# Kernel tuning notes

Measured on AMD Instinct MI355X. Metric: run time of the kernel, lower is better.

## Reference

```python
import jax, jax.numpy as jnp
import numpy as np

B, T, H, NH, K = 8, 1024, 1024, 16, 3
HD = H // NH
EPS = 1e-5


def _ln(x, g, b):
    m = jnp.mean(x, axis=-1, keepdims=True)
    v = jnp.mean((x - m) ** 2, axis=-1, keepdims=True)
    return (x - m) * jax.lax.rsqrt(v + EPS) * g + b


def _ffn(x, g, b, w1, b1, w2, b2):
    h = jax.nn.gelu(_ln(x, g, b) @ w1 + b1, approximate=False)
    return h @ w2 + b2


def setup_inputs() -> dict:
    key = jax.random.key(0)
    ks = jax.random.split(key, 10)
    s = 0.02
    d = {}
    d['x'] = jax.random.normal(ks[0], (B, T, H), jnp.float32)
    d['ln1_g'] = jnp.ones((H,), jnp.float32); d['ln1_b'] = jnp.zeros((H,), jnp.float32)
    d['ffn1_w1'] = jax.random.normal(ks[1], (H, 2 * H), jnp.float32) * s
    d['ffn1_b1'] = jnp.zeros((2 * H,), jnp.float32)
    d['ffn1_w2'] = jax.random.normal(ks[2], (2 * H, H), jnp.float32) * s
    d['ffn1_b2'] = jnp.zeros((H,), jnp.float32)
    d['an_g'] = jnp.ones((H,), jnp.float32); d['an_b'] = jnp.zeros((H,), jnp.float32)
    d['qkv_w'] = jax.random.normal(ks[3], (H, 3 * H), jnp.float32) * s
    d['qkv_b'] = jnp.zeros((3 * H,), jnp.float32)
    d['out_w'] = jax.random.normal(ks[4], (H, H), jnp.float32) * s
    d['out_b'] = jnp.zeros((H,), jnp.float32)
    d['cn_g'] = jnp.ones((H,), jnp.float32); d['cn_b'] = jnp.zeros((H,), jnp.float32)
    d['dw_k'] = jax.random.normal(ks[5], (H, 1, K), jnp.float32) * s  # depthwise [O,I/g,K]
    d['dw_b'] = jnp.zeros((H,), jnp.float32)
    d['pw_w'] = jax.random.normal(ks[6], (H, H), jnp.float32) * s  # pointwise [out,in]
    d['pw_b'] = jnp.zeros((H,), jnp.float32)
    d['ln2_g'] = jnp.ones((H,), jnp.float32); d['ln2_b'] = jnp.zeros((H,), jnp.float32)
    d['ffn2_w1'] = jax.random.normal(ks[7], (H, 2 * H), jnp.float32) * s
    d['ffn2_b1'] = jnp.zeros((2 * H,), jnp.float32)
    d['ffn2_w2'] = jax.random.normal(ks[8], (2 * H, H), jnp.float32) * s
    d['ffn2_b2'] = jnp.zeros((H,), jnp.float32)
    return d


def reference(x, ln1_g, ln1_b, ffn1_w1, ffn1_b1, ffn1_w2, ffn1_b2,
              an_g, an_b, qkv_w, qkv_b, out_w, out_b,
              cn_g, cn_b, dw_k, dw_b, pw_w, pw_b,
              ln2_g, ln2_b, ffn2_w1, ffn2_b1, ffn2_w2, ffn2_b2):
    # macaron FFN 1
    x = x + 0.5 * _ffn(x, ln1_g, ln1_b, ffn1_w1, ffn1_b1, ffn1_w2, ffn1_b2)

    # causal self-attention (pre-norm)
    h = _ln(x, an_g, an_b)
    qkv = (h @ qkv_w + qkv_b).reshape(B, T, 3, NH, HD)
    q, k, v = qkv[:, :, 0], qkv[:, :, 1], qkv[:, :, 2]  # [B,T,NH,HD]
    scale = 1.0 / np.sqrt(HD).astype(np.float32)
    scores = jnp.einsum('bqhd,bkhd->bhqk', q, k) * scale  # [B,NH,T,T]
    causal = jnp.tril(jnp.ones((T, T), dtype=bool))
    scores = jnp.where(causal[None, None], scores, -jnp.inf)
    attn = jax.nn.softmax(scores, axis=-1)
    o = jnp.einsum('bhqk,bkhd->bqhd', attn, v).reshape(B, T, H)
    x = x + (o @ out_w + out_b)

    # conv module: LN -> causal depthwise conv(k=3) -> GELU -> pointwise conv
    c = _ln(x, cn_g, cn_b).transpose(0, 2, 1)  # [B,H,T]
    c = jnp.pad(c, ((0, 0), (0, 0), (K - 1, 0)))  # causal left pad
    c = jax.lax.conv_general_dilated(
        c, dw_k, window_strides=(1,), padding='VALID',
        dimension_numbers=('NCH', 'OIH', 'NCH'), feature_group_count=H)
    c = c + dw_b[None, :, None]
    c = jax.nn.gelu(c, approximate=False)
    c = jnp.einsum('oc,bct->bot', pw_w, c) + pw_b[None, :, None]  # 1x1 conv
    x = x + c.transpose(0, 2, 1)

    # macaron FFN 2
    x = x + 0.5 * _ffn(x, ln2_g, ln2_b, ffn2_w1, ffn2_b1, ffn2_w2, ffn2_b2)
    return x
```

## Files before the change

kernel.cpp:

```cpp
#include <hip/hip_runtime.h>
#include <hip/hip_bf16.h>
#include <math.h>

typedef __bf16 bf16;
typedef __bf16 bf16x8 __attribute__((ext_vector_type(8)));
typedef float  f32x4  __attribute__((ext_vector_type(4)));

#define B_   8
#define T_   1024
#define H_   1024
#define MTOK (B_ * T_)

static __device__ __forceinline__ float gelu_f(float x) {
    return 0.5f * x * (1.0f + erff(x * 0.70710678118654752f));
}

static __device__ __forceinline__ void async16(const bf16* g, bf16* l) {
    __builtin_amdgcn_global_load_lds(
        (const __attribute__((address_space(1))) void*)g,
        (__attribute__((address_space(3))) void*)l, 16, 0, 0);
}

__global__ __launch_bounds__(256)
void transpose_cast_k(const float* __restrict__ in, bf16* __restrict__ out,
                      int Kd, int Nd)
{
    __shared__ float tile[32][33];
    int n0 = blockIdx.x * 32;
    int k0 = blockIdx.y * 32;
    int tx = threadIdx.x & 31, ty = threadIdx.x >> 5;
#pragma unroll
    for (int i = 0; i < 32; i += 8)
        tile[ty + i][tx] = in[(size_t)(k0 + ty + i) * Nd + n0 + tx];
    __syncthreads();
#pragma unroll
    for (int i = 0; i < 32; i += 8)
        out[(size_t)(n0 + ty + i) * Kd + k0 + tx] = (bf16)tile[tx][ty + i];
}

__global__ __launch_bounds__(256)
void cast_k(const float* __restrict__ in, bf16* __restrict__ out)
{
    int i = blockIdx.x * 256 + threadIdx.x;
    float4 v = ((const float4*)in)[i];
    bf16* o = out + (size_t)i * 4;
    o[0] = (bf16)v.x; o[1] = (bf16)v.y; o[2] = (bf16)v.z; o[3] = (bf16)v.w;
}

__global__ __launch_bounds__(256)
void transpose_v_k(const bf16* __restrict__ qkv, bf16* __restrict__ vt)
{
    __shared__ bf16 tile[64][72];
    const int t0 = blockIdx.x * 64;
    const int bh = blockIdx.y;
    const int b = bh >> 4, h = bh & 15;
    const int tid = threadIdx.x;
#pragma unroll
    for (int i = 0; i < 2; i++) {
        int c = tid + i * 256;
        int row = c >> 3, ch = (c & 7) << 3;
        *(bf16x8*)(&tile[row][ch]) =
            *(const bf16x8*)(&qkv[(size_t)(b * T_ + t0 + row) * 3072 + 2048 + h * 64 + ch]);
    }
    __syncthreads();
#pragma unroll
    for (int i = 0; i < 2; i++) {
        int c = tid + i * 256;
        int hd = c >> 3, tc = (c & 7) << 3;
        bf16x8 v;
#pragma unroll
        for (int j = 0; j < 8; j++) v[j] = tile[tc + j][hd];
        *(bf16x8*)(&vt[((size_t)bh * 64 + hd) * T_ + t0 + tc]) = v;
    }
}

__global__ __launch_bounds__(256)
void ln_k(const float* __restrict__ x, const float* __restrict__ g,
          const float* __restrict__ b, bf16* __restrict__ out)
{
    int row = blockIdx.x;
    float4 v = ((const float4*)(x + (size_t)row * H_))[threadIdx.x];
    float s  = v.x + v.y + v.z + v.w;
    float s2 = v.x * v.x + v.y * v.y + v.z * v.z + v.w * v.w;
#pragma unroll
    for (int off = 32; off > 0; off >>= 1) {
        s  += __shfl_down(s, off);
        s2 += __shfl_down(s2, off);
    }
    __shared__ float red[8];
    int wave = threadIdx.x >> 6, lane = threadIdx.x & 63;
    if (lane == 0) { red[wave] = s; red[wave + 4] = s2; }
    __syncthreads();
    s  = red[0] + red[1] + red[2] + red[3];
    s2 = red[4] + red[5] + red[6] + red[7];
    float mean = s * (1.0f / H_);
    float var  = s2 * (1.0f / H_) - mean * mean;
    float rstd = rsqrtf(var + 1e-5f);
    int c = threadIdx.x * 4;
    float4 gv = *(const float4*)(g + c);
    float4 bv = *(const float4*)(b + c);
    bf16* o = out + (size_t)row * H_ + c;
    o[0] = (bf16)((v.x - mean) * rstd * gv.x + bv.x);
    o[1] = (bf16)((v.y - mean) * rstd * gv.y + bv.y);
    o[2] = (bf16)((v.z - mean) * rstd * gv.z + bv.z);
    o[3] = (bf16)((v.w - mean) * rstd * gv.w + bv.w);
}

__global__ __launch_bounds__(256)
void dwconv_k(const bf16* __restrict__ cl, const float* __restrict__ kw,
              const float* __restrict__ kb, bf16* __restrict__ out)
{
    size_t idx = (size_t)blockIdx.x * 256 + threadIdx.x;
    int ch = (int)(idx & (H_ - 1));
    int t  = (int)((idx >> 10) & (T_ - 1));
    float acc = kb[ch];
    float w0 = kw[ch * 3 + 0], w1 = kw[ch * 3 + 1], w2 = kw[ch * 3 + 2];
    acc += (float)cl[idx] * w2;
    if (t >= 1) acc += (float)cl[idx - H_] * w1;
    if (t >= 2) acc += (float)cl[idx - 2 * H_] * w0;
    out[idx] = (bf16)gelu_f(acc);
}

template<int EPI>
__global__ __launch_bounds__(256)
void gemm_k(const bf16* __restrict__ A, const bf16* __restrict__ WT,
            const float* __restrict__ bias, const float* __restrict__ res,
            float* __restrict__ outF, bf16* __restrict__ outB,
            int N, int K)
{
    __shared__ __align__(16) bf16 As[2][128 * 32];
    __shared__ __align__(16) bf16 Bs[2][128 * 32];
    const int tid  = threadIdx.x;
    const int wave = tid >> 6;
    const int lane = tid & 63;
    const int quad = lane >> 4;
    const int lr   = lane & 15;
    const int bm = blockIdx.x * 128;
    const int bn = blockIdx.y * 128;
    const int wm = (wave & 1) * 64;
    const int wn = (wave >> 1) * 64;

    const int crow = lane >> 2;
    const int ccol = (lane & 3) << 3;

    f32x4 acc[4][4];
#pragma unroll
    for (int mi = 0; mi < 4; mi++)
#pragma unroll
        for (int ni = 0; ni < 4; ni++)
#pragma unroll
            for (int r = 0; r < 4; r++) acc[mi][ni][r] = 0.f;

    for (int k0 = 0; k0 < K; k0 += 64) {
#pragma unroll
        for (int half = 0; half < 2; half++) {
#pragma unroll
            for (int t = 0; t < 2; t++) {
                const int c = wave * 2 + t;
                async16(&A[(size_t)(bm + c * 16 + crow) * K + k0 + half * 32 + ccol],
                        &As[half][c * 512]);
                async16(&WT[(size_t)(bn + c * 16 + crow) * K + k0 + half * 32 + ccol],
                        &Bs[half][c * 512]);
            }
        }
        __syncthreads();
#pragma unroll
        for (int half = 0; half < 2; half++) {
            bf16x8 af[4], bfr[4];
#pragma unroll
            for (int mi = 0; mi < 4; mi++)
                af[mi] = *(const bf16x8*)(&As[half][(wm + mi * 16 + lr) * 32 + quad * 8]);
#pragma unroll
            for (int ni = 0; ni < 4; ni++)
                bfr[ni] = *(const bf16x8*)(&Bs[half][(wn + ni * 16 + lr) * 32 + quad * 8]);
#pragma unroll
            for (int mi = 0; mi < 4; mi++)
#pragma unroll
                for (int ni = 0; ni < 4; ni++)
                    acc[mi][ni] = __builtin_amdgcn_mfma_f32_16x16x32_bf16(
                        af[mi], bfr[ni], acc[mi][ni], 0, 0, 0);
        }
        __syncthreads();
    }

#pragma unroll
    for (int mi = 0; mi < 4; mi++) {
#pragma unroll
        for (int ni = 0; ni < 4; ni++) {
            int col = bn + wn + ni * 16 + lr;
            float bv = bias[col];
#pragma unroll
            for (int r = 0; r < 4; r++) {
                int row = bm + wm + mi * 16 + quad * 4 + r;
                size_t idx = (size_t)row * N + col;
                float v = acc[mi][ni][r] + bv;
                if (EPI == 0)      outB[idx] = (bf16)gelu_f(v);
                else if (EPI == 1) outB[idx] = (bf16)v;
                else if (EPI == 2) outF[idx] = v + res[idx];
                else               outF[idx] = res[idx] + 0.5f * v;
            }
        }
    }
}

template<int EPI>
__global__ __launch_bounds__(256)
void gemm64_k(const bf16* __restrict__ A, const bf16* __restrict__ WT,
              const float* __restrict__ bias, const float* __restrict__ res,
              float* __restrict__ outF, bf16* __restrict__ outB,
              int N, int K)
{
    __shared__ __align__(16) bf16 As[2][64 * 32];
    __shared__ __align__(16) bf16 Bs[2][128 * 32];
    const int tid  = threadIdx.x;
    const int wave = tid >> 6;
    const int lane = tid & 63;
    const int quad = lane >> 4;
    const int lr   = lane & 15;
    const int bm = blockIdx.x * 64;
    const int bn = blockIdx.y * 128;
    const int wm = (wave & 1) * 32;
    const int wn = (wave >> 1) * 64;

    const int crow = lane >> 2;
    const int ccol = (lane & 3) << 3;

    f32x4 acc[2][4];
#pragma unroll
    for (int mi = 0; mi < 2; mi++)
#pragma unroll
        for (int ni = 0; ni < 4; ni++)
#pragma unroll
            for (int r = 0; r < 4; r++) acc[mi][ni][r] = 0.f;

    for (int k0 = 0; k0 < K; k0 += 64) {
#pragma unroll
        for (int half = 0; half < 2; half++) {
            async16(&A[(size_t)(bm + wave * 16 + crow) * K + k0 + half * 32 + ccol],
                    &As[half][wave * 512]);
#pragma unroll
            for (int t = 0; t < 2; t++) {
                const int c = wave * 2 + t;
                async16(&WT[(size_t)(bn + c * 16 + crow) * K + k0 + half * 32 + ccol],
                        &Bs[half][c * 512]);
            }
        }
        __syncthreads();
#pragma unroll
        for (int half = 0; half < 2; half++) {
            bf16x8 af[2], bfr[4];
#pragma unroll
            for (int mi = 0; mi < 2; mi++)
                af[mi] = *(const bf16x8*)(&As[half][(wm + mi * 16 + lr) * 32 + quad * 8]);
#pragma unroll
            for (int ni = 0; ni < 4; ni++)
                bfr[ni] = *(const bf16x8*)(&Bs[half][(wn + ni * 16 + lr) * 32 + quad * 8]);
#pragma unroll
            for (int mi = 0; mi < 2; mi++)
#pragma unroll
                for (int ni = 0; ni < 4; ni++)
                    acc[mi][ni] = __builtin_amdgcn_mfma_f32_16x16x32_bf16(
                        af[mi], bfr[ni], acc[mi][ni], 0, 0, 0);
        }
        __syncthreads();
    }

#pragma unroll
    for (int mi = 0; mi < 2; mi++) {
#pragma unroll
        for (int ni = 0; ni < 4; ni++) {
            int col = bn + wn + ni * 16 + lr;
            float bv = bias[col];
#pragma unroll
            for (int r = 0; r < 4; r++) {
                int row = bm + wm + mi * 16 + quad * 4 + r;
                size_t idx = (size_t)row * N + col;
                float v = acc[mi][ni][r] + bv;
                if (EPI == 0)      outB[idx] = (bf16)gelu_f(v);
                else if (EPI == 1) outB[idx] = (bf16)v;
                else if (EPI == 2) outF[idx] = v + res[idx];
                else               outF[idx] = res[idx] + 0.5f * v;
            }
        }
    }
}

__global__ __launch_bounds__(256)
void attn_k(const bf16* __restrict__ qkv, const bf16* __restrict__ vt,
            bf16* __restrict__ o)
{
    const int B0 = blockIdx.x;
    const int bh = blockIdx.y;
    const int b = bh >> 4, h = bh & 15;
    const int tid  = threadIdx.x;
    const int wave = tid >> 6, lane = tid & 63;
    const int quad = lane >> 4, lr = lane & 15;

    __shared__ __align__(16) bf16 Ks[2][64 * 32];
    __shared__ __align__(16) bf16 Vs[2][64 * 32];
    __shared__ __align__(16) bf16 Ps[4][16 * 72];

    const int crow = lane >> 2;
    const int ccol = (lane & 3) << 3;

    const int qa = B0 * 128 + wave * 16;
    const int qb = qa + 64;

    bf16x8 qfa[2], qfb[2];
    {
        const size_t ra = ((size_t)(b * T_ + qa + lr)) * 3072 + h * 64;
        const size_t rb = ((size_t)(b * T_ + qb + lr)) * 3072 + h * 64;
        qfa[0] = *(const bf16x8*)(&qkv[ra + quad * 8]);
        qfa[1] = *(const bf16x8*)(&qkv[ra + 32 + quad * 8]);
        qfb[0] = *(const bf16x8*)(&qkv[rb + quad * 8]);
        qfb[1] = *(const bf16x8*)(&qkv[rb + 32 + quad * 8]);
#pragma unroll
        for (int j = 0; j < 8; j++) {
            qfa[0][j] = (bf16)((float)qfa[0][j] * 0.125f);
            qfa[1][j] = (bf16)((float)qfa[1][j] * 0.125f);
            qfb[0][j] = (bf16)((float)qfb[0][j] * 0.125f);
            qfb[1][j] = (bf16)((float)qfb[1][j] * 0.125f);
        }
    }

    f32x4 oa[4], ob[4];
    float la[4], lb[4];
#pragma unroll
    for (int ni = 0; ni < 4; ni++)
#pragma unroll
        for (int r = 0; r < 4; r++) { oa[ni][r] = 0.f; ob[ni][r] = 0.f; }
#pragma unroll
    for (int r = 0; r < 4; r++) { la[r] = 0.f; lb[r] = 0.f; }

    const size_t kbase = (size_t)b * T_ * 3072 + 1024 + h * 64;
    const size_t vbase = (size_t)bh * 64 * T_;

    auto stripe = [&](const bf16x8 (&qf)[2], f32x4 (&oacc)[4], float (&lsum)[4],
                      int q0, int kcol0, bool diag) {
        bf16x8 kf0[4], kf1[4];
#pragma unroll
        for (int ni = 0; ni < 4; ni++) {
            kf0[ni] = *(const bf16x8*)(&Ks[0][(ni * 16 + lr) * 32 + quad * 8]);
            kf1[ni] = *(const bf16x8*)(&Ks[1][(ni * 16 + lr) * 32 + quad * 8]);
        }
        f32x4 sv[4];
#pragma unroll
        for (int ni = 0; ni < 4; ni++) {
            f32x4 t;
#pragma unroll
            for (int r = 0; r < 4; r++) t[r] = 0.f;
            t = __builtin_amdgcn_mfma_f32_16x16x32_bf16(qf[0], kf0[ni], t, 0, 0, 0);
            t = __builtin_amdgcn_mfma_f32_16x16x32_bf16(qf[1], kf1[ni], t, 0, 0, 0);
            sv[ni] = t;
        }
        if (diag) {
#pragma unroll
            for (int ni = 0; ni < 4; ni++)
#pragma unroll
                for (int r = 0; r < 4; r++)
                    if (kcol0 + ni * 16 + lr > q0 + quad * 4 + r)
                        sv[ni][r] = -INFINITY;
        }
#pragma unroll
        for (int ni = 0; ni < 4; ni++)
#pragma unroll
            for (int r = 0; r < 4; r++) {
                float p = __expf(sv[ni][r]);
                lsum[r] += p;
                Ps[wave][(quad * 4 + r) * 72 + ni * 16 + lr] = (bf16)p;
            }
        bf16x8 pf0 = *(const bf16x8*)(&Ps[wave][lr * 72 + quad * 8]);
        bf16x8 pf1 = *(const bf16x8*)(&Ps[wave][lr * 72 + 32 + quad * 8]);
#pragma unroll
        for (int ni = 0; ni < 4; ni++) {
            bf16x8 vf0 = *(const bf16x8*)(&Vs[0][(ni * 16 + lr) * 32 + quad * 8]);
            bf16x8 vf1 = *(const bf16x8*)(&Vs[1][(ni * 16 + lr) * 32 + quad * 8]);
            oacc[ni] = __builtin_amdgcn_mfma_f32_16x16x32_bf16(pf0, vf0, oacc[ni], 0, 0, 0);
            oacc[ni] = __builtin_amdgcn_mfma_f32_16x16x32_bf16(pf1, vf1, oacc[ni], 0, 0, 0);
        }
    };

    const int ktmax = 2 * B0 + 1;
    for (int kt = 0; kt <= ktmax; kt++) {
#pragma unroll
        for (int half = 0; half < 2; half++) {
            async16(&qkv[kbase + (size_t)(kt * 64 + wave * 16 + crow) * 3072 + half * 32 + ccol],
                    &Ks[half][wave * 512]);
            async16(&vt[vbase + (size_t)(wave * 16 + crow) * T_ + kt * 64 + half * 32 + ccol],
                    &Vs[half][wave * 512]);
        }
        __syncthreads();
        if (kt <= 2 * B0)
            stripe(qfa, oa, la, qa, kt * 64, kt == 2 * B0);
        stripe(qfb, ob, lb, qb, kt * 64, kt == ktmax);
        __syncthreads();
    }

#pragma unroll
    for (int off = 1; off < 16; off <<= 1)
#pragma unroll
        for (int r = 0; r < 4; r++) {
            la[r] += __shfl_xor(la[r], off);
            lb[r] += __shfl_xor(lb[r], off);
        }

#pragma unroll
    for (int r = 0; r < 4; r++) {
        float inva = 1.0f / la[r], invb = 1.0f / lb[r];
        int ga = qa + quad * 4 + r, gb = qb + quad * 4 + r;
#pragma unroll
        for (int ni = 0; ni < 4; ni++) {
            o[((size_t)(b * T_ + ga)) * H_ + h * 64 + ni * 16 + lr] = (bf16)(oa[ni][r] * inva);
            o[((size_t)(b * T_ + gb)) * H_ + h * 64 + ni * 16 + lr] = (bf16)(ob[ni][r] * invb);
        }
    }
}

extern "C" void kernel_launch(void* const* d_in, const int* in_sizes, int n_in,
                              void* d_out, int out_size, void* d_ws, size_t ws_size,
                              hipStream_t stream)
{
    const float* x_in  = (const float*)d_in[0];
    const float* ln1_g = (const float*)d_in[1];
    const float* ln1_b = (const float*)d_in[2];
    const float* f1w1  = (const float*)d_in[3];
    const float* f1b1  = (const float*)d_in[4];
    const float* f1w2  = (const float*)d_in[5];
    const float* f1b2  = (const float*)d_in[6];
    const float* an_g  = (const float*)d_in[7];
    const float* an_b  = (const float*)d_in[8];
    const float* qkv_w = (const float*)d_in[9];
    const float* qkv_b = (const float*)d_in[10];
    const float* out_w = (const float*)d_in[11];
    const float* out_b = (const float*)d_in[12];
    const float* cn_g  = (const float*)d_in[13];
    const float* cn_b  = (const float*)d_in[14];
    const float* dw_k  = (const float*)d_in[15];
    const float* dw_b  = (const float*)d_in[16];
    const float* pw_w  = (const float*)d_in[17];
    const float* pw_b  = (const float*)d_in[18];
    const float* ln2_g = (const float*)d_in[19];
    const float* ln2_b = (const float*)d_in[20];
    const float* f2w1  = (const float*)d_in[21];
    const float* f2b1  = (const float*)d_in[22];
    const float* f2w2  = (const float*)d_in[23];
    const float* f2b2  = (const float*)d_in[24];
    float* outp = (float*)d_out;

    char* ws = (char*)d_ws;
    size_t off = 0;
    auto alloc = [&](size_t bytes) {
        char* p = ws + off;
        off += (bytes + 255) & ~(size_t)255;
        return p;
    };
    bf16* w1T_1 = (bf16*)alloc(2048ULL * 1024 * 2);
    bf16* w2T_1 = (bf16*)alloc(1024ULL * 2048 * 2);
    bf16* qkvT  = (bf16*)alloc(3072ULL * 1024 * 2);
    bf16* outT  = (bf16*)alloc(1024ULL * 1024 * 2);
    bf16* pwB   = (bf16*)alloc(1024ULL * 1024 * 2);
    bf16* w1T_2 = (bf16*)alloc(2048ULL * 1024 * 2);
    bf16* w2T_2 = (bf16*)alloc(1024ULL * 2048 * 2);
    bf16* bufa  = (bf16*)alloc((size_t)MTOK * 1024 * 2);
    bf16* gbuf  = (bf16*)alloc((size_t)MTOK * 1024 * 2);
    bf16* hid   = (bf16*)alloc((size_t)MTOK * 3072 * 2);
    float* xw   = (float*)alloc((size_t)MTOK * 1024 * 4);
    bf16* vt    = gbuf;

    transpose_cast_k<<<dim3(64, 32), 256, 0, stream>>>(f1w1, w1T_1, 1024, 2048);
    transpose_cast_k<<<dim3(32, 64), 256, 0, stream>>>(f1w2, w2T_1, 2048, 1024);
    transpose_cast_k<<<dim3(96, 32), 256, 0, stream>>>(qkv_w, qkvT, 1024, 3072);
    transpose_cast_k<<<dim3(32, 32), 256, 0, stream>>>(out_w, outT, 1024, 1024);
    transpose_cast_k<<<dim3(64, 32), 256, 0, stream>>>(f2w1, w1T_2, 1024, 2048);
    transpose_cast_k<<<dim3(32, 64), 256, 0, stream>>>(f2w2, w2T_2, 2048, 1024);
    cast_k<<<1024, 256, 0, stream>>>(pw_w, pwB);

    ln_k<<<MTOK, 256, 0, stream>>>(x_in, ln1_g, ln1_b, bufa);
    gemm_k<0><<<dim3(64, 16), 256, 0, stream>>>(bufa, w1T_1, f1b1, nullptr, nullptr, hid, 2048, 1024);
    gemm64_k<3><<<dim3(128, 8), 256, 0, stream>>>(hid, w2T_1, f1b2, x_in, xw, nullptr, 1024, 2048);

    ln_k<<<MTOK, 256, 0, stream>>>(xw, an_g, an_b, bufa);
    gemm_k<1><<<dim3(64, 24), 256, 0, stream>>>(bufa, qkvT, qkv_b, nullptr, nullptr, hid, 3072, 1024);
    transpose_v_k<<<dim3(16, 128), 256, 0, stream>>>(hid, vt);
    attn_k<<<dim3(8, 128), 256, 0, stream>>>(hid, vt, bufa);
    gemm64_k<2><<<dim3(128, 8), 256, 0, stream>>>(bufa, outT, out_b, xw, xw, nullptr, 1024, 1024);

    ln_k<<<MTOK, 256, 0, stream>>>(xw, cn_g, cn_b, bufa);
    dwconv_k<<<MTOK * 1024 / 256, 256, 0, stream>>>(bufa, dw_k, dw_b, gbuf);
    gemm64_k<2><<<dim3(128, 8), 256, 0, stream>>>(gbuf, pwB, pw_b, xw, xw, nullptr, 1024, 1024);

    ln_k<<<MTOK, 256, 0, stream>>>(xw, ln2_g, ln2_b, bufa);
    gemm_k<0><<<dim3(64, 16), 256, 0, stream>>>(bufa, w1T_2, f2b1, nullptr, nullptr, hid, 2048, 1024);
    gemm64_k<3><<<dim3(128, 8), 256, 0, stream>>>(hid, w2T_2, f2b2, xw, outp, nullptr, 1024, 2048);
}
```

Baseline: 685.0 us.

## Double-buffer LDS tiles in GEMM and attention kernels to overlap loads with MFMA

The GEMM kernels now stage K-slices of 32 into alternating LDS buffers, issuing the async global-to-LDS copy for the next slice before computing on the current one. This drops one barrier per step and aims to hide global load latency behind MFMA work. The attention kernel likewise double-buffers its K and V tiles and hoists their fragment loads out of the per-stripe code so both query stripes reuse them. In exchange, the GEMMs take smaller per-iteration steps with more iterations, and attention uses more LDS and registers, which may lower occupancy. There is also no explicit wait on the async LDS loads before the following barrier, so correctness depends on how the barrier orders those loads.

```diff
diff --git a/kernel.cpp b/kernel.cpp
--- a/kernel.cpp
+++ b/kernel.cpp
@@ -143,6 +143,15 @@
     const int crow = lane >> 2;
     const int ccol = (lane & 3) << 3;
 
+    auto stage = [&](int k0, int buf) {
+#pragma unroll
+        for (int t = 0; t < 2; t++) {
+            const int c = wave * 2 + t;
+            async16(&A[(size_t)(bm + c * 16 + crow) * K + k0 + ccol], &As[buf][c * 512]);
+            async16(&WT[(size_t)(bn + c * 16 + crow) * K + k0 + ccol], &Bs[buf][c * 512]);
+        }
+    };
+
     f32x4 acc[4][4];
 #pragma unroll
     for (int mi = 0; mi < 4; mi++)
@@ -151,35 +160,26 @@
 #pragma unroll
             for (int r = 0; r < 4; r++) acc[mi][ni][r] = 0.f;
 
-    for (int k0 = 0; k0 < K; k0 += 64) {
-#pragma unroll
-        for (int half = 0; half < 2; half++) {
-#pragma unroll
-            for (int t = 0; t < 2; t++) {
-                const int c = wave * 2 + t;
-                async16(&A[(size_t)(bm + c * 16 + crow) * K + k0 + half * 32 + ccol],
-                        &As[half][c * 512]);
-                async16(&WT[(size_t)(bn + c * 16 + crow) * K + k0 + half * 32 + ccol],
-                        &Bs[half][c * 512]);
-            }
-        }
-        __syncthreads();
-#pragma unroll
-        for (int half = 0; half < 2; half++) {
-            bf16x8 af[4], bfr[4];
-#pragma unroll
-            for (int mi = 0; mi < 4; mi++)
-                af[mi] = *(const bf16x8*)(&As[half][(wm + mi * 16 + lr) * 32 + quad * 8]);
+    stage(0, 0);
+    __syncthreads();
+    const int nk = K >> 5;
+    for (int ki = 0; ki < nk; ki++) {
+        const int cur = ki & 1;
+        if (ki + 1 < nk) stage((ki + 1) << 5, cur ^ 1);
+
+        bf16x8 af[4], bfr[4];
+#pragma unroll
+        for (int mi = 0; mi < 4; mi++)
+            af[mi] = *(const bf16x8*)(&As[cur][(wm + mi * 16 + lr) * 32 + quad * 8]);
+#pragma unroll
+        for (int ni = 0; ni < 4; ni++)
+            bfr[ni] = *(const bf16x8*)(&Bs[cur][(wn + ni * 16 + lr) * 32 + quad * 8]);
+#pragma unroll
+        for (int mi = 0; mi < 4; mi++)
 #pragma unroll
             for (int ni = 0; ni < 4; ni++)
-                bfr[ni] = *(const bf16x8*)(&Bs[half][(wn + ni * 16 + lr) * 32 + quad * 8]);
-#pragma unroll
-            for (int mi = 0; mi < 4; mi++)
-#pragma unroll
-                for (int ni = 0; ni < 4; ni++)
-                    acc[mi][ni] = __builtin_amdgcn_mfma_f32_16x16x32_bf16(
-                        af[mi], bfr[ni], acc[mi][ni], 0, 0, 0);
-        }
+                acc[mi][ni] = __builtin_amdgcn_mfma_f32_16x16x32_bf16(
+                    af[mi], bfr[ni], acc[mi][ni], 0, 0, 0);
         __syncthreads();
     }
 
@@ -225,6 +225,15 @@
     const int crow = lane >> 2;
     const int ccol = (lane & 3) << 3;
 
+    auto stage = [&](int k0, int buf) {
+        async16(&A[(size_t)(bm + wave * 16 + crow) * K + k0 + ccol], &As[buf][wave * 512]);
+#pragma unroll
+        for (int t = 0; t < 2; t++) {
+            const int c = wave * 2 + t;
+            async16(&WT[(size_t)(bn + c * 16 + crow) * K + k0 + ccol], &Bs[buf][c * 512]);
+        }
+    };
+
     f32x4 acc[2][4];
 #pragma unroll
     for (int mi = 0; mi < 2; mi++)
@@ -233,35 +242,26 @@
 #pragma unroll
             for (int r = 0; r < 4; r++) acc[mi][ni][r] = 0.f;
 
-    for (int k0 = 0; k0 < K; k0 += 64) {
-#pragma unroll
-        for (int half = 0; half < 2; half++) {
-            async16(&A[(size_t)(bm + wave * 16 + crow) * K + k0 + half * 32 + ccol],
-                    &As[half][wave * 512]);
-#pragma unroll
-            for (int t = 0; t < 2; t++) {
-                const int c = wave * 2 + t;
-                async16(&WT[(size_t)(bn + c * 16 + crow) * K + k0 + half * 32 + ccol],
-                        &Bs[half][c * 512]);
-            }
-        }
-        __syncthreads();
-#pragma unroll
-        for (int half = 0; half < 2; half++) {
-            bf16x8 af[2], bfr[4];
-#pragma unroll
-            for (int mi = 0; mi < 2; mi++)
-                af[mi] = *(const bf16x8*)(&As[half][(wm + mi * 16 + lr) * 32 + quad * 8]);
+    stage(0, 0);
+    __syncthreads();
+    const int nk = K >> 5;
+    for (int ki = 0; ki < nk; ki++) {
+        const int cur = ki & 1;
+        if (ki + 1 < nk) stage((ki + 1) << 5, cur ^ 1);
+
+        bf16x8 af[2], bfr[4];
+#pragma unroll
+        for (int mi = 0; mi < 2; mi++)
+            af[mi] = *(const bf16x8*)(&As[cur][(wm + mi * 16 + lr) * 32 + quad * 8]);
+#pragma unroll
+        for (int ni = 0; ni < 4; ni++)
+            bfr[ni] = *(const bf16x8*)(&Bs[cur][(wn + ni * 16 + lr) * 32 + quad * 8]);
+#pragma unroll
+        for (int mi = 0; mi < 2; mi++)
 #pragma unroll
             for (int ni = 0; ni < 4; ni++)
-                bfr[ni] = *(const bf16x8*)(&Bs[half][(wn + ni * 16 + lr) * 32 + quad * 8]);
-#pragma unroll
-            for (int mi = 0; mi < 2; mi++)
-#pragma unroll
-                for (int ni = 0; ni < 4; ni++)
-                    acc[mi][ni] = __builtin_amdgcn_mfma_f32_16x16x32_bf16(
-                        af[mi], bfr[ni], acc[mi][ni], 0, 0, 0);
-        }
+                acc[mi][ni] = __builtin_amdgcn_mfma_f32_16x16x32_bf16(
+                    af[mi], bfr[ni], acc[mi][ni], 0, 0, 0);
         __syncthreads();
     }
 
@@ -296,8 +296,8 @@
     const int wave = tid >> 6, lane = tid & 63;
     const int quad = lane >> 4, lr = lane & 15;
 
-    __shared__ __align__(16) bf16 Ks[2][64 * 32];
-    __shared__ __align__(16) bf16 Vs[2][64 * 32];
+    __shared__ __align__(16) bf16 Ks[2][2][64 * 32];
+    __shared__ __align__(16) bf16 Vs[2][2][64 * 32];
     __shared__ __align__(16) bf16 Ps[4][16 * 72];
 
     const int crow = lane >> 2;
@@ -335,64 +335,73 @@
     const size_t kbase = (size_t)b * T_ * 3072 + 1024 + h * 64;
     const size_t vbase = (size_t)bh * 64 * T_;
 
-    auto stripe = [&](const bf16x8 (&qf)[2], f32x4 (&oacc)[4], float (&lsum)[4],
-                      int q0, int kcol0, bool diag) {
-        bf16x8 kf0[4], kf1[4];
-#pragma unroll
-        for (int ni = 0; ni < 4; ni++) {
-            kf0[ni] = *(const bf16x8*)(&Ks[0][(ni * 16 + lr) * 32 + quad * 8]);
-            kf1[ni] = *(const bf16x8*)(&Ks[1][(ni * 16 + lr) * 32 + quad * 8]);
-        }
-        f32x4 sv[4];
-#pragma unroll
-        for (int ni = 0; ni < 4; ni++) {
-            f32x4 t;
-#pragma unroll
-            for (int r = 0; r < 4; r++) t[r] = 0.f;
-            t = __builtin_amdgcn_mfma_f32_16x16x32_bf16(qf[0], kf0[ni], t, 0, 0, 0);
-            t = __builtin_amdgcn_mfma_f32_16x16x32_bf16(qf[1], kf1[ni], t, 0, 0, 0);
-            sv[ni] = t;
-        }
-        if (diag) {
-#pragma unroll
-            for (int ni = 0; ni < 4; ni++)
-#pragma unroll
-                for (int r = 0; r < 4; r++)
-                    if (kcol0 + ni * 16 + lr > q0 + quad * 4 + r)
-                        sv[ni][r] = -INFINITY;
-        }
-#pragma unroll
-        for (int ni = 0; ni < 4; ni++)
-#pragma unroll
-            for (int r = 0; r < 4; r++) {
-                float p = __expf(sv[ni][r]);
-                lsum[r] += p;
-                Ps[wave][(quad * 4 + r) * 72 + ni * 16 + lr] = (bf16)p;
-            }
-        bf16x8 pf0 = *(const bf16x8*)(&Ps[wave][lr * 72 + quad * 8]);
-        bf16x8 pf1 = *(const bf16x8*)(&Ps[wave][lr * 72 + 32 + quad * 8]);
-#pragma unroll
-        for (int ni = 0; ni < 4; ni++) {
-            bf16x8 vf0 = *(const bf16x8*)(&Vs[0][(ni * 16 + lr) * 32 + quad * 8]);
-            bf16x8 vf1 = *(const bf16x8*)(&Vs[1][(ni * 16 + lr) * 32 + quad * 8]);
-            oacc[ni] = __builtin_amdgcn_mfma_f32_16x16x32_bf16(pf0, vf0, oacc[ni], 0, 0, 0);
-            oacc[ni] = __builtin_amdgcn_mfma_f32_16x16x32_bf16(pf1, vf1, oacc[ni], 0, 0, 0);
-        }
-    };
-
-    const int ktmax = 2 * B0 + 1;
-    for (int kt = 0; kt <= ktmax; kt++) {
+    auto stage = [&](int kt, int buf) {
 #pragma unroll
         for (int half = 0; half < 2; half++) {
             async16(&qkv[kbase + (size_t)(kt * 64 + wave * 16 + crow) * 3072 + half * 32 + ccol],
-                    &Ks[half][wave * 512]);
+                    &Ks[buf][half][wave * 512]);
             async16(&vt[vbase + (size_t)(wave * 16 + crow) * T_ + kt * 64 + half * 32 + ccol],
-                    &Vs[half][wave * 512]);
-        }
-        __syncthreads();
+                    &Vs[buf][half][wave * 512]);
+        }
+    };
+
+    const int ktmax = 2 * B0 + 1;
+    stage(0, 0);
+    __syncthreads();
+
+    for (int kt = 0; kt <= ktmax; kt++) {
+        const int cur = kt & 1;
+        if (kt < ktmax) stage(kt + 1, cur ^ 1);
+
+        bf16x8 kf[4][2], vf[4][2];
+#pragma unroll
+        for (int ni = 0; ni < 4; ni++) {
+            kf[ni][0] = *(const bf16x8*)(&Ks[cur][0][(ni * 16 + lr) * 32 + quad * 8]);
+            kf[ni][1] = *(const bf16x8*)(&Ks[cur][1][(ni * 16 + lr) * 32 + quad * 8]);
+            vf[ni][0] = *(const bf16x8*)(&Vs[cur][0][(ni * 16 + lr) * 32 + quad * 8]);
+            vf[ni][1] = *(const bf16x8*)(&Vs[cur][1][(ni * 16 + lr) * 32 + quad * 8]);
+        }
+
+        auto stripe = [&](const bf16x8 (&qf)[2], f32x4 (&oacc)[4], float (&lsum)[4],
+                          int q0, bool diag) {
+            f32x4 sv[4];
+#pragma unroll
+            for (int ni = 0; ni < 4; ni++) {
+                f32x4 t;
+#pragma unroll
+                for (int r = 0; r < 4; r++) t[r] = 0.f;
+                t = __builtin_amdgcn_mfma_f32_16x16x32_bf16(qf[0], kf[ni][0], t, 0, 0, 0);
+                t = __builtin_amdgcn_mfma_f32_16x16x32_bf16(qf[1], kf[ni][1], t, 0, 0, 0);
+                sv[ni] = t;
+            }
+            if (diag) {
+#pragma unroll
+                for (int ni = 0; ni < 4; ni++)
+#pragma unroll
+                    for (int r = 0; r < 4; r++)
+                        if (kt * 64 + ni * 16 + lr > q0 + quad * 4 + r)
+                            sv[ni][r] = -INFINITY;
+            }
+#pragma unroll
+            for (int ni = 0; ni < 4; ni++)
+#pragma unroll
+                for (int r = 0; r < 4; r++) {
+                    float p = __expf(sv[ni][r]);
+                    lsum[r] += p;
+                    Ps[wave][(quad * 4 + r) * 72 + ni * 16 + lr] = (bf16)p;
+                }
+            bf16x8 pf0 = *(const bf16x8*)(&Ps[wave][lr * 72 + quad * 8]);
+            bf16x8 pf1 = *(const bf16x8*)(&Ps[wave][lr * 72 + 32 + quad * 8]);
+#pragma unroll
+            for (int ni = 0; ni < 4; ni++) {
+                oacc[ni] = __builtin_amdgcn_mfma_f32_16x16x32_bf16(pf0, vf[ni][0], oacc[ni], 0, 0, 0);
+                oacc[ni] = __builtin_amdgcn_mfma_f32_16x16x32_bf16(pf1, vf[ni][1], oacc[ni], 0, 0, 0);
+            }
+        };
+
         if (kt <= 2 * B0)
-            stripe(qfa, oa, la, qa, kt * 64, kt == 2 * B0);
-        stripe(qfb, ob, lb, qb, kt * 64, kt == ktmax);
+            stripe(qfa, oa, la, qa, kt == 2 * B0);
+        stripe(qfb, ob, lb, qb, kt == ktmax);
         __syncthreads();
     }
 
```

After: 683.0 us. About the same (-0.3%).

## Replace LDS-staged GEMM tiles with direct register loads and software pipelining

Applied to the files above, without the earlier changes.

Both GEMM kernels stop staging A/B tiles in LDS through async global-to-LDS loads and barriers. Each wave now loads its MFMA fragments straight from global memory into registers, double- or quad-buffered so the next k-slice is fetched while the current one is computed. This removes the LDS round trip and the __syncthreads stalls, but gives up intra-block data sharing: each wave re-reads rows that other waves also need, so global and L2 traffic rises and register pressure grows. The attention loop's barrier also moves to the top of the iteration, dropping the redundant trailing sync.

```diff
diff --git a/kernel.cpp b/kernel.cpp
--- a/kernel.cpp
+++ b/kernel.cpp
@@ -123,13 +123,11 @@
 
 template<int EPI>
 __global__ __launch_bounds__(256)
-void gemm_k(const bf16* __restrict__ A, const bf16* __restrict__ WT,
+void gemm_r(const bf16* __restrict__ A, const bf16* __restrict__ WT,
             const float* __restrict__ bias, const float* __restrict__ res,
             float* __restrict__ outF, bf16* __restrict__ outB,
             int N, int K)
 {
-    __shared__ __align__(16) bf16 As[2][128 * 32];
-    __shared__ __align__(16) bf16 Bs[2][128 * 32];
     const int tid  = threadIdx.x;
     const int wave = tid >> 6;
     const int lane = tid & 63;
@@ -140,8 +138,9 @@
     const int wm = (wave & 1) * 64;
     const int wn = (wave >> 1) * 64;
 
-    const int crow = lane >> 2;
-    const int ccol = (lane & 3) << 3;
+    const bf16* pA = A  + (size_t)(bm + wm + lr) * K + quad * 8;
+    const bf16* pB = WT + (size_t)(bn + wn + lr) * K + quad * 8;
+    const size_t rs = (size_t)16 * K;
 
     f32x4 acc[4][4];
 #pragma unroll
@@ -151,36 +150,30 @@
 #pragma unroll
             for (int r = 0; r < 4; r++) acc[mi][ni][r] = 0.f;
 
-    for (int k0 = 0; k0 < K; k0 += 64) {
-#pragma unroll
-        for (int half = 0; half < 2; half++) {
-#pragma unroll
-            for (int t = 0; t < 2; t++) {
-                const int c = wave * 2 + t;
-                async16(&A[(size_t)(bm + c * 16 + crow) * K + k0 + half * 32 + ccol],
-                        &As[half][c * 512]);
-                async16(&WT[(size_t)(bn + c * 16 + crow) * K + k0 + half * 32 + ccol],
-                        &Bs[half][c * 512]);
-            }
-        }
-        __syncthreads();
-#pragma unroll
-        for (int half = 0; half < 2; half++) {
-            bf16x8 af[4], bfr[4];
-#pragma unroll
-            for (int mi = 0; mi < 4; mi++)
-                af[mi] = *(const bf16x8*)(&As[half][(wm + mi * 16 + lr) * 32 + quad * 8]);
+    bf16x8 a0[4], b0[4], a1[4], b1[4];
+
+    auto ld = [&](int k, bf16x8 (&af)[4], bf16x8 (&bf)[4]) {
+#pragma unroll
+        for (int i = 0; i < 4; i++) {
+            af[i] = *(const bf16x8*)(pA + i * rs + k);
+            bf[i] = *(const bf16x8*)(pB + i * rs + k);
+        }
+    };
+    auto comp = [&](bf16x8 (&af)[4], bf16x8 (&bf)[4]) {
+#pragma unroll
+        for (int mi = 0; mi < 4; mi++)
 #pragma unroll
             for (int ni = 0; ni < 4; ni++)
-                bfr[ni] = *(const bf16x8*)(&Bs[half][(wn + ni * 16 + lr) * 32 + quad * 8]);
-#pragma unroll
-            for (int mi = 0; mi < 4; mi++)
-#pragma unroll
-                for (int ni = 0; ni < 4; ni++)
-                    acc[mi][ni] = __builtin_amdgcn_mfma_f32_16x16x32_bf16(
-                        af[mi], bfr[ni], acc[mi][ni], 0, 0, 0);
-        }
-        __syncthreads();
+                acc[mi][ni] = __builtin_amdgcn_mfma_f32_16x16x32_bf16(
+                    af[mi], bf[ni], acc[mi][ni], 0, 0, 0);
+    };
+
+    ld(0, a0, b0);
+    for (int k = 0; k < K; k += 64) {
+        ld(k + 32, a1, b1);
+        comp(a0, b0);
+        if (k + 64 < K) ld(k + 64, a0, b0);
+        comp(a1, b1);
     }
 
 #pragma unroll
@@ -205,13 +198,11 @@
 
 template<int EPI>
 __global__ __launch_bounds__(256)
-void gemm64_k(const bf16* __restrict__ A, const bf16* __restrict__ WT,
+void gemm64_r(const bf16* __restrict__ A, const bf16* __restrict__ WT,
               const float* __restrict__ bias, const float* __restrict__ res,
               float* __restrict__ outF, bf16* __restrict__ outB,
               int N, int K)
 {
-    __shared__ __align__(16) bf16 As[2][64 * 32];
-    __shared__ __align__(16) bf16 Bs[2][128 * 32];
     const int tid  = threadIdx.x;
     const int wave = tid >> 6;
     const int lane = tid & 63;
@@ -222,8 +213,9 @@
     const int wm = (wave & 1) * 32;
     const int wn = (wave >> 1) * 64;
 
-    const int crow = lane >> 2;
-    const int ccol = (lane & 3) << 3;
+    const bf16* pA = A  + (size_t)(bm + wm + lr) * K + quad * 8;
+    const bf16* pB = WT + (size_t)(bn + wn + lr) * K + quad * 8;
+    const size_t rs = (size_t)16 * K;
 
     f32x4 acc[2][4];
 #pragma unroll
@@ -233,36 +225,32 @@
 #pragma unroll
             for (int r = 0; r < 4; r++) acc[mi][ni][r] = 0.f;
 
-    for (int k0 = 0; k0 < K; k0 += 64) {
-#pragma unroll
-        for (int half = 0; half < 2; half++) {
-            async16(&A[(size_t)(bm + wave * 16 + crow) * K + k0 + half * 32 + ccol],
-                    &As[half][wave * 512]);
-#pragma unroll
-            for (int t = 0; t < 2; t++) {
-                const int c = wave * 2 + t;
-                async16(&WT[(size_t)(bn + c * 16 + crow) * K + k0 + half * 32 + ccol],
-                        &Bs[half][c * 512]);
-            }
-        }
-        __syncthreads();
-#pragma unroll
-        for (int half = 0; half < 2; half++) {
-            bf16x8 af[2], bfr[4];
-#pragma unroll
-            for (int mi = 0; mi < 2; mi++)
-                af[mi] = *(const bf16x8*)(&As[half][(wm + mi * 16 + lr) * 32 + quad * 8]);
+    bf16x8 a[4][2], b[4][4];
+
+    auto ld = [&](int k, int s) {
+        if (k < K) {
+#pragma unroll
+            for (int i = 0; i < 2; i++) a[s][i] = *(const bf16x8*)(pA + i * rs + k);
+#pragma unroll
+            for (int i = 0; i < 4; i++) b[s][i] = *(const bf16x8*)(pB + i * rs + k);
+        }
+    };
+    auto comp = [&](int s) {
+#pragma unroll
+        for (int mi = 0; mi < 2; mi++)
 #pragma unroll
             for (int ni = 0; ni < 4; ni++)
-                bfr[ni] = *(const bf16x8*)(&Bs[half][(wn + ni * 16 + lr) * 32 + quad * 8]);
-#pragma unroll
-            for (int mi = 0; mi < 2; mi++)
-#pragma unroll
-                for (int ni = 0; ni < 4; ni++)
-                    acc[mi][ni] = __builtin_amdgcn_mfma_f32_16x16x32_bf16(
-                        af[mi], bfr[ni], acc[mi][ni], 0, 0, 0);
-        }
-        __syncthreads();
+                acc[mi][ni] = __builtin_amdgcn_mfma_f32_16x16x32_bf16(
+                    a[s][mi], b[s][ni], acc[mi][ni], 0, 0, 0);
+    };
+
+    ld(0, 0);
+    ld(32, 1);
+    for (int k = 0; k < K; k += 128) {
+        ld(k + 64, 2);  comp(0);
+        ld(k + 96, 3);  comp(1);
+        ld(k + 128, 0); comp(2);
+        ld(k + 160, 1); comp(3);
     }
 
 #pragma unroll
@@ -382,6 +370,7 @@
 
     const int ktmax = 2 * B0 + 1;
     for (int kt = 0; kt <= ktmax; kt++) {
+        __syncthreads();
 #pragma unroll
         for (int half = 0; half < 2; half++) {
             async16(&qkv[kbase + (size_t)(kt * 64 + wave * 16 + crow) * 3072 + half * 32 + ccol],
@@ -393,7 +382,6 @@
         if (kt <= 2 * B0)
             stripe(qfa, oa, la, qa, kt * 64, kt == 2 * B0);
         stripe(qfb, ob, lb, qb, kt * 64, kt == ktmax);
-        __syncthreads();
     }
 
 #pragma unroll
@@ -476,20 +464,20 @@
     cast_k<<<1024, 256, 0, stream>>>(pw_w, pwB);
 
     ln_k<<<MTOK, 256, 0, stream>>>(x_in, ln1_g, ln1_b, bufa);
-    gemm_k<0><<<dim3(64, 16), 256, 0, stream>>>(bufa, w1T_1, f1b1, nullptr, nullptr, hid, 2048, 1024);
-    gemm64_k<3><<<dim3(128, 8), 256, 0, stream>>>(hid, w2T_1, f1b2, x_in, xw, nullptr, 1024, 2048);
+    gemm_r<0><<<dim3(64, 16), 256, 0, stream>>>(bufa, w1T_1, f1b1, nullptr, nullptr, hid, 2048, 1024);
+    gemm64_r<3><<<dim3(128, 8), 256, 0, stream>>>(hid, w2T_1, f1b2, x_in, xw, nullptr, 1024, 2048);
 
     ln_k<<<MTOK, 256, 0, stream>>>(xw, an_g, an_b, bufa);
-    gemm_k<1><<<dim3(64, 24), 256, 0, stream>>>(bufa, qkvT, qkv_b, nullptr, nullptr, hid, 3072, 1024);
+    gemm_r<1><<<dim3(64, 24), 256, 0, stream>>>(bufa, qkvT, qkv_b, nullptr, nullptr, hid, 3072, 1024);
     transpose_v_k<<<dim3(16, 128), 256, 0, stream>>>(hid, vt);
     attn_k<<<dim3(8, 128), 256, 0, stream>>>(hid, vt, bufa);
-    gemm64_k<2><<<dim3(128, 8), 256, 0, stream>>>(bufa, outT, out_b, xw, xw, nullptr, 1024, 1024);
+    gemm64_r<2><<<dim3(128, 8), 256, 0, stream>>>(bufa, outT, out_b, xw, xw, nullptr, 1024, 1024);
 
     ln_k<<<MTOK, 256, 0, stream>>>(xw, cn_g, cn_b, bufa);
     dwconv_k<<<MTOK * 1024 / 256, 256, 0, stream>>>(bufa, dw_k, dw_b, gbuf);
-    gemm64_k<2><<<dim3(128, 8), 256, 0, stream>>>(gbuf, pwB, pw_b, xw, xw, nullptr, 1024, 1024);
+    gemm64_r<2><<<dim3(128, 8), 256, 0, stream>>>(gbuf, pwB, pw_b, xw, xw, nullptr, 1024, 1024);
 
     ln_k<<<MTOK, 256, 0, stream>>>(xw, ln2_g, ln2_b, bufa);
-    gemm_k<0><<<dim3(64, 16), 256, 0, stream>>>(bufa, w1T_2, f2b1, nullptr, nullptr, hid, 2048, 1024);
-    gemm64_k<3><<<dim3(128, 8), 256, 0, stream>>>(hid, w2T_2, f2b2, xw, outp, nullptr, 1024, 2048);
-}
+    gemm_r<0><<<dim3(64, 16), 256, 0, stream>>>(bufa, w1T_2, f2b1, nullptr, nullptr, hid, 2048, 1024);
+    gemm64_r<3><<<dim3(128, 8), 256, 0, stream>>>(hid, w2T_2, f2b2, xw, outp, nullptr, 1024, 2048);
+}
```

New measurement: 1.273 ms. +85.8%, slower.
